# Kernel tuning notes

Measured on AMD Instinct MI355X. Metric: run time of the kernel, lower is better.

Reference implementation:

```python
import math
import jax, jax.numpy as jnp
import numpy as np

D_MODEL = 1024
N_HEADS = 16
D_K = D_MODEL // N_HEADS


def _build_neighbours(n_heads):
    # Mirrors LatticeMultiHeadAttention._build_neighbours for a (4,4)-style lattice.
    side = int(math.sqrt(n_heads))
    cols = side + 1 if side * side < n_heads else side
    positions = [divmod(i, cols) for i in range(n_heads)]
    pos_map = {p: j for j, p in enumerate(positions)}
    nb_idx = np.full((n_heads, 8), -1, dtype=np.int64)
    nb_w = np.zeros((n_heads, 8), dtype=np.float32)
    for i, (r, c) in enumerate(positions):
        k = 0
        for dr in (-1, 0, 1):
            for dc in (-1, 0, 1):
                if dr == 0 and dc == 0:
                    continue
                j = pos_map.get((r + dr, c + dc))
                if j is not None and k < 8:
                    nb_idx[i, k] = j
                    nb_w[i, k] = math.exp(-math.hypot(dr, dc))
                    k += 1
    return nb_idx, nb_w


def _phase_biases(coupling):
    # Sequential Kuramoto phase update: head h uses neighbor phases already
    # updated for heads < h (exactly as the torch per-head loop mutates buffers).
    H = coupling.shape[0]
    nb_idx, nb_w = _build_neighbours(H)
    phases = [jnp.asarray(0.0, coupling.dtype) for _ in range(H)]
    two_pi = 2.0 * math.pi
    for h in range(H):
        force = jnp.asarray(0.0, coupling.dtype)
        for k in range(8):
            j = int(nb_idx[h, k])
            if j >= 0:
                force = force + jnp.asarray(nb_w[h, k], coupling.dtype) * jnp.sin(phases[j] - phases[h])
        intrinsic = 1.0 + 0.1 * h
        new_phase = (phases[h] + 0.01 * (intrinsic + coupling[h] * force)) % two_pi
        phases[h] = new_phase
    return 0.1 * jnp.cos(jnp.stack(phases))  # [H] per-head scalar bias


def setup_inputs() -> dict:
    key = jax.random.key(0)
    ks = jax.random.split(key, 9)
    B, L = 2, 2048
    std = 0.02
    return {
        "query": jax.random.normal(ks[0], (B, L, D_MODEL), jnp.float32),
        "key": jax.random.normal(ks[1], (B, L, D_MODEL), jnp.float32),
        "value": jax.random.normal(ks[2], (B, L, D_MODEL), jnp.float32),
        "Wq": std * jax.random.normal(ks[3], (N_HEADS, D_MODEL, D_K), jnp.float32),
        "Wk": std * jax.random.normal(ks[4], (N_HEADS, D_MODEL, D_K), jnp.float32),
        "Wv": std * jax.random.normal(ks[5], (N_HEADS, D_MODEL, D_K), jnp.float32),
        "out_w": std * jax.random.normal(ks[6], (D_MODEL, D_MODEL), jnp.float32),
        "out_b": jnp.zeros((D_MODEL,), jnp.float32),
        "coupling": 0.1 * jnp.ones((N_HEADS,), jnp.float32),
    }


def reference(query, key, value, Wq, Wk, Wv, out_w, out_b, coupling):
    d_k = Wq.shape[-1]
    Q = jnp.einsum("bld,hdk->bhlk", query, Wq)
    K = jnp.einsum("bld,hdk->bhlk", key, Wk)
    V = jnp.einsum("bld,hdk->bhlk", value, Wv)
    scale = jnp.asarray(math.sqrt(float(d_k)), query.dtype)
    scores = jnp.einsum("bhlk,bhmk->bhlm", Q, K) / scale
    bias = _phase_biases(coupling)  # [H]
    scores = scores + bias[None, :, None, None]
    attn = jax.nn.softmax(scores, axis=-1)
    ctx = jnp.einsum("bhlm,bhmk->bhlk", attn, V)
    B, H, L, _ = ctx.shape
    out = ctx.transpose(0, 2, 1, 3).reshape(B, L, H * d_k)  # concat heads
    return out @ out_w + out_b
```

## Files before the change

kernel.cpp:

```cpp
#include <hip/hip_runtime.h>
#include <cstdint>

typedef uint16_t u16;
typedef __attribute__((ext_vector_type(8))) short bf16x8;
typedef __attribute__((ext_vector_type(4))) short bf16x4;
typedef __attribute__((ext_vector_type(4))) float f32x4;

#define QSCALE 0.18033688011112042f

struct Ptr3 { const float* a; const float* b; const float* c; };

__device__ __forceinline__ u16 f2bf(float x) {
  union { float f; uint32_t u; } v; v.f = x;
  uint32_t r = (v.u + 0x7fffu + ((v.u >> 16) & 1u)) >> 16;
  return (u16)r;
}

__device__ __forceinline__ void async16(void* lds, const void* g) {
  __builtin_amdgcn_global_load_lds((const __attribute__((address_space(1))) void*)g,
                                   (__attribute__((address_space(3))) void*)lds, 16, 0, 0);
}

__global__ __launch_bounds__(256) void k_cast3(Ptr3 in, u16* __restrict__ out) {
  const int z = blockIdx.y;
  const float* p = z == 0 ? in.a : (z == 1 ? in.b : in.c);
  int i = blockIdx.x * 256 + threadIdx.x;
  float4 v = ((const float4*)p)[i];
  bf16x4 o;
  o[0] = (short)f2bf(v.x); o[1] = (short)f2bf(v.y);
  o[2] = (short)f2bf(v.z); o[3] = (short)f2bf(v.w);
  *(bf16x4*)(out + (long)z * 4194304 + (long)i * 4) = o;
}

__global__ __launch_bounds__(256) void k_transpose_all(Ptr3 w, const float* __restrict__ ow,
                                                       u16* __restrict__ wt,
                                                       u16* __restrict__ wto) {
  __shared__ u16 tile[64 * 65];
  const int t = threadIdx.x;
  const int bx = blockIdx.x;
  const float* in;
  long in_base, out_base;
  int rstr, r0, c0;
  u16* outp;
  if (bx < 768) {
    int z = bx >> 4;
    r0 = (bx & 15) * 64; c0 = 0;
    in = (z < 16) ? w.a : (z < 32 ? w.b : w.c);
    in_base = (long)(z & 15) * 65536;
    out_base = (long)z * 65536;
    rstr = 64; outp = wt;
  } else {
    int idx = bx - 768;
    r0 = (idx >> 4) * 64; c0 = (idx & 15) * 64;
    in = ow; in_base = 0; out_base = 0;
    rstr = 1024; outp = wto;
  }
  for (int e = t; e < 4096; e += 256) {
    int rr = e >> 6, cc = e & 63;
    tile[rr * 65 + cc] = f2bf(in[in_base + (long)(r0 + rr) * rstr + c0 + cc]);
  }
  __syncthreads();
  for (int s = t; s < 512; s += 256) {
    int cc = s >> 3, r8 = (s & 7) << 3;
    bf16x8 p;
    #pragma unroll
    for (int j = 0; j < 8; ++j) p[j] = (short)tile[(r8 + j) * 65 + cc];
    *(bf16x8*)(outp + out_base + (long)(c0 + cc) * 1024 + r0 + r8) = p;
  }
}

__global__ __launch_bounds__(256) void k_gemm_qkv(const u16* __restrict__ A0,
                                                  const u16* __restrict__ B0,
                                                  u16* __restrict__ C0,
                                                  u16* __restrict__ Vt, float scale0) {
  __shared__ __align__(16) u16 As[128 * 32];
  __shared__ __align__(16) u16 Bs[128 * 32];
  __shared__ u16 T[128 * 130];
  const int z = blockIdx.z;
  const u16* A = A0 + (long)z * 4194304;
  const u16* Bt = B0 + (long)z * 1048576;
  const int t = threadIdx.x, lane = t & 63, quad = lane >> 4, l16 = lane & 15;
  const int wave = t >> 6, wy = wave >> 1, wx = wave & 1;
  const int m0 = blockIdx.y * 128, n0 = blockIdx.x * 128;
  const int wbase = t & 192;
  f32x4 acc[4][4] = {};
  for (int k0 = 0; k0 < 1024; k0 += 32) {
    __syncthreads();
    #pragma unroll
    for (int i = 0; i < 2; ++i) {
      int sb = i * 256 + wbase;
      int s = sb + lane;
      int row = s >> 2, c = s & 3;
      async16(As + sb * 8, A + (long)(m0 + row) * 1024 + k0 + c * 8);
      async16(Bs + sb * 8, Bt + (long)(n0 + row) * 1024 + k0 + c * 8);
    }
    __syncthreads();
    bf16x8 af[4], bfr[4];
    #pragma unroll
    for (int mt = 0; mt < 4; ++mt)
      af[mt] = *(const bf16x8*)(As + (wy * 64 + mt * 16 + l16) * 32 + quad * 8);
    #pragma unroll
    for (int nt = 0; nt < 4; ++nt)
      bfr[nt] = *(const bf16x8*)(Bs + (wx * 64 + nt * 16 + l16) * 32 + quad * 8);
    #pragma unroll
    for (int mt = 0; mt < 4; ++mt)
      #pragma unroll
      for (int nt = 0; nt < 4; ++nt)
        acc[mt][nt] = __builtin_amdgcn_mfma_f32_16x16x32_bf16(af[mt], bfr[nt], acc[mt][nt], 0, 0, 0);
  }
  if (z < 2) {
    u16* C = C0 + (long)z * 4194304;
    const float scale = z ? 1.0f : scale0;
    #pragma unroll
    for (int mt = 0; mt < 4; ++mt)
      #pragma unroll
      for (int nt = 0; nt < 4; ++nt) {
        int col = n0 + wx * 64 + nt * 16 + l16;
        #pragma unroll
        for (int r = 0; r < 4; ++r) {
          int row = m0 + wy * 64 + mt * 16 + quad * 4 + r;
          C[(long)row * 1024 + col] = f2bf(acc[mt][nt][r] * scale);
        }
      }
  } else {
    #pragma unroll
    for (int mt = 0; mt < 4; ++mt)
      #pragma unroll
      for (int nt = 0; nt < 4; ++nt) {
        int cc = wx * 64 + nt * 16 + l16;
        #pragma unroll
        for (int r = 0; r < 4; ++r)
          T[(wy * 64 + mt * 16 + quad * 4 + r) * 130 + cc] = f2bf(acc[mt][nt][r]);
      }
    __syncthreads();
    const int h0 = blockIdx.x * 2, bb = m0 >> 11, lb = m0 & 2047;
    #pragma unroll
    for (int i = 0; i < 8; ++i) {
      int s = t + i * 256;
      int c = s >> 4, l0 = (s & 15) * 8;
      bf16x8 p;
      #pragma unroll
      for (int j = 0; j < 8; ++j) p[j] = (short)T[(l0 + j) * 130 + c];
      *(bf16x8*)(Vt + (long)(bb * 16 + h0 + (c >> 6)) * 131072 +
                 (long)(c & 63) * 2048 + lb + l0) = p;
    }
  }
}

__global__ __launch_bounds__(256) void k_gemm_out(const u16* __restrict__ A,
                                                  const u16* __restrict__ Bt,
                                                  float* __restrict__ C,
                                                  const float* __restrict__ bias) {
  __shared__ __align__(16) u16 As[128 * 32];
  __shared__ __align__(16) u16 Bs[64 * 32];
  const int t = threadIdx.x, lane = t & 63, quad = lane >> 4, l16 = lane & 15;
  const int wave = t >> 6;
  const int m0 = blockIdx.y * 128, n0 = blockIdx.x * 64;
  const int wbase = t & 192;
  f32x4 acc[2][4] = {};
  for (int k0 = 0; k0 < 1024; k0 += 32) {
    __syncthreads();
    #pragma unroll
    for (int i = 0; i < 2; ++i) {
      int sb = i * 256 + wbase;
      int s = sb + lane;
      int row = s >> 2, c = s & 3;
      async16(As + sb * 8, A + (long)(m0 + row) * 1024 + k0 + c * 8);
    }
    {
      int s = t;
      int row = s >> 2, c = s & 3;
      async16(Bs + wbase * 8, Bt + (long)(n0 + row) * 1024 + k0 + c * 8);
    }
    __syncthreads();
    bf16x8 af[2], bfr[4];
    #pragma unroll
    for (int mt = 0; mt < 2; ++mt)
      af[mt] = *(const bf16x8*)(As + (wave * 32 + mt * 16 + l16) * 32 + quad * 8);
    #pragma unroll
    for (int nt = 0; nt < 4; ++nt)
      bfr[nt] = *(const bf16x8*)(Bs + (nt * 16 + l16) * 32 + quad * 8);
    #pragma unroll
    for (int mt = 0; mt < 2; ++mt)
      #pragma unroll
      for (int nt = 0; nt < 4; ++nt)
        acc[mt][nt] = __builtin_amdgcn_mfma_f32_16x16x32_bf16(af[mt], bfr[nt], acc[mt][nt], 0, 0, 0);
  }
  #pragma unroll
  for (int mt = 0; mt < 2; ++mt)
    #pragma unroll
    for (int nt = 0; nt < 4; ++nt) {
      int col = n0 + nt * 16 + l16;
      #pragma unroll
      for (int r = 0; r < 4; ++r) {
        int row = m0 + wave * 32 + mt * 16 + quad * 4 + r;
        C[(long)row * 1024 + col] = acc[mt][nt][r] + bias[col];
      }
    }
}

__global__ __launch_bounds__(512, 2) void k_flash(const u16* __restrict__ Qp,
                                                  const u16* __restrict__ Kp,
                                                  const u16* __restrict__ Vt,
                                                  u16* __restrict__ ctx) {
  __shared__ __align__(16) u16 qs[256 * 64];
  __shared__ __align__(16) u16 ks[64 * 72];
  __shared__ __align__(16) u16 vs[64 * 72];
  const int t = threadIdx.x, lane = t & 63, quad = lane >> 4, l16 = lane & 15;
  const int wave = t >> 6;
  const int bh = blockIdx.x & 31, b = bh >> 4, h = bh & 15;
  const int q0 = (blockIdx.x >> 5) * 256;
  const long gkbase = (long)b * 2097152 + h * 64;
  const long gvbase = (long)bh * 131072;
  const int srow = t >> 3, sc = t & 7;

  {
    long gq = (long)(b * 2048 + q0) * 1024 + h * 64;
    #pragma unroll
    for (int i = 0; i < 4; ++i) {
      int s = i * 512 + t;
      int row = s >> 3, pos = s & 7, c = pos ^ (row & 7);
      async16(qs + (long)s * 8, Qp + gq + (long)row * 1024 + c * 8);
    }
  }
  bf16x8 kreg = *(const bf16x8*)(Kp + gkbase + (long)srow * 1024 + sc * 8);
  bf16x8 vreg = *(const bf16x8*)(Vt + gvbase + (long)srow * 2048 + sc * 8);
  __syncthreads();

  bf16x8 qf[2][2];
  #pragma unroll
  for (int msub = 0; msub < 2; ++msub)
    #pragma unroll
    for (int kh = 0; kh < 2; ++kh) {
      int m = wave * 32 + msub * 16 + l16;
      int pos = (kh * 4 + quad) ^ (m & 7);
      qf[msub][kh] = *(const bf16x8*)(qs + m * 64 + pos * 8);
    }
  *(bf16x8*)(ks + srow * 72 + sc * 8) = kreg;
  *(bf16x8*)(vs + srow * 72 + sc * 8) = vreg;
  __syncthreads();

  u16* pw = qs + wave * 1152;

  float lsum[2][4] = {};
  f32x4 o[2][4] = {};

  for (int kt = 0; kt < 32; ++kt) {
    if (kt < 31) {
      int kv0 = (kt + 1) * 64;
      kreg = *(const bf16x8*)(Kp + gkbase + (long)(kv0 + srow) * 1024 + sc * 8);
      vreg = *(const bf16x8*)(Vt + gvbase + kv0 + (long)srow * 2048 + sc * 8);
    }

    bf16x8 kf[4][2], vf[4][2];
    #pragma unroll
    for (int nt = 0; nt < 4; ++nt)
      #pragma unroll
      for (int kh = 0; kh < 2; ++kh) {
        kf[nt][kh] = *(const bf16x8*)(ks + (nt * 16 + l16) * 72 + kh * 32 + quad * 8);
        vf[nt][kh] = *(const bf16x8*)(vs + (nt * 16 + l16) * 72 + kh * 32 + quad * 8);
      }

    #pragma unroll
    for (int msub = 0; msub < 2; ++msub) {
      #pragma unroll
      for (int nt = 0; nt < 4; ++nt) {
        f32x4 a = {};
        #pragma unroll
        for (int kh = 0; kh < 2; ++kh)
          a = __builtin_amdgcn_mfma_f32_16x16x32_bf16(qf[msub][kh], kf[nt][kh], a, 0, 0, 0);
        #pragma unroll
        for (int r = 0; r < 4; ++r) {
          float e = __builtin_amdgcn_exp2f(a[r]);
          lsum[msub][r] += e;
          pw[(quad * 4 + r) * 72 + nt * 16 + l16] = f2bf(e);
        }
      }
      #pragma unroll
      for (int kh = 0; kh < 2; ++kh) {
        bf16x8 pa = *(const bf16x8*)(pw + l16 * 72 + kh * 32 + quad * 8);
        #pragma unroll
        for (int nt = 0; nt < 4; ++nt)
          o[msub][nt] = __builtin_amdgcn_mfma_f32_16x16x32_bf16(pa, vf[nt][kh], o[msub][nt], 0, 0, 0);
      }
    }

    __syncthreads();
    if (kt < 31) {
      *(bf16x8*)(ks + srow * 72 + sc * 8) = kreg;
      *(bf16x8*)(vs + srow * 72 + sc * 8) = vreg;
    }
    __syncthreads();
  }

  #pragma unroll
  for (int msub = 0; msub < 2; ++msub)
    #pragma unroll
    for (int r = 0; r < 4; ++r) {
      float l = lsum[msub][r];
      #pragma unroll
      for (int d = 1; d < 16; d <<= 1) l += __shfl_xor(l, d);
      lsum[msub][r] = 1.0f / l;
    }
  #pragma unroll
  for (int msub = 0; msub < 2; ++msub)
    #pragma unroll
    for (int nt = 0; nt < 4; ++nt)
      #pragma unroll
      for (int r = 0; r < 4; ++r) {
        int q = q0 + wave * 32 + msub * 16 + quad * 4 + r;
        long idx = (long)(b * 2048 + q) * 1024 + h * 64 + nt * 16 + l16;
        ctx[idx] = f2bf(o[msub][nt][r] * lsum[msub][r]);
      }
}

extern "C" void kernel_launch(void* const* d_in, const int* in_sizes, int n_in,
                              void* d_out, int out_size, void* d_ws, size_t ws_size,
                              hipStream_t stream) {
  const float* query = (const float*)d_in[0];
  const float* key   = (const float*)d_in[1];
  const float* value = (const float*)d_in[2];
  const float* Wq    = (const float*)d_in[3];
  const float* Wk    = (const float*)d_in[4];
  const float* Wv    = (const float*)d_in[5];
  const float* out_w = (const float*)d_in[6];
  const float* out_b = (const float*)d_in[7];
  float* out = (float*)d_out;

  char* ws = (char*)d_ws;
  size_t off = 0;
  auto alloc = [&](size_t bytes) {
    void* p = ws + off;
    off += (bytes + 255) & ~(size_t)255;
    return p;
  };
  u16* qb  = (u16*)alloc(4096L * 1024 * 2);
  u16* kb  = (u16*)alloc(4096L * 1024 * 2);
  u16* vb  = (u16*)alloc(4096L * 1024 * 2);
  u16* wtq = (u16*)alloc(1024L * 1024 * 2);
  u16* wtk = (u16*)alloc(1024L * 1024 * 2);
  u16* wtv = (u16*)alloc(1024L * 1024 * 2);
  u16* wto = (u16*)alloc(1024L * 1024 * 2);
  u16* Qp  = (u16*)alloc(4096L * 1024 * 2);
  u16* Kp  = (u16*)alloc(4096L * 1024 * 2);
  u16* Vtb = (u16*)alloc(4096L * 1024 * 2);
  u16* ctx = qb;
  (void)kb; (void)vb; (void)wtk; (void)wtv; (void)Kp;

  k_cast3<<<dim3(4096, 3), 256, 0, stream>>>(Ptr3{query, key, value}, qb);

  k_transpose_all<<<1024, 256, 0, stream>>>(Ptr3{Wq, Wk, Wv}, out_w, wtq, wto);

  k_gemm_qkv<<<dim3(8, 32, 3), 256, 0, stream>>>(qb, wtq, Qp, Vtb, QSCALE);

  k_flash<<<256, 512, 0, stream>>>(Qp, Kp, Vtb, ctx);

  k_gemm_out<<<dim3(16, 32), 256, 0, stream>>>(ctx, wto, out, out_b);
}
```

Baseline: 246.3 us.

## Merge prep kernels, widen QKV GEMM k-tile with XOR swizzle, use packed bf16 conversion

Merges the input cast and weight transpose into one prep launch to cut a kernel launch. The QKV GEMM now stages a k-depth of 64 per iteration with an XOR-swizzled LDS layout, which halves barrier count and avoids bank conflicts. Its LDS buffers are shared with the transpose scratch area, which needs an extra barrier. Float-to-bf16 conversion uses the hardware packed-convert builtin when it is available, in the GEMM epilogues, the flash softmax P write and the ctx store. Risk: the packed convert's rounding may differ slightly from the manual round-to-nearest-even code.

New measurement: 234.4 us. 1.05x faster.

```diff
diff --git a/kernel.cpp b/kernel.cpp
--- a/kernel.cpp
+++ b/kernel.cpp
@@ -16,48 +16,63 @@
   return (u16)r;
 }
 
+#if __has_builtin(__builtin_amdgcn_cvt_pk_bf16_f32)
+typedef __bf16 bf2_t __attribute__((ext_vector_type(2)));
+__device__ __forceinline__ uint32_t pkbf(float a, float b) {
+  bf2_t v = __builtin_amdgcn_cvt_pk_bf16_f32(a, b);
+  uint32_t u;
+  __builtin_memcpy(&u, &v, 4);
+  return u;
+}
+#else
+__device__ __forceinline__ uint32_t pkbf(float a, float b) {
+  return (uint32_t)f2bf(a) | ((uint32_t)f2bf(b) << 16);
+}
+#endif
+
 __device__ __forceinline__ void async16(void* lds, const void* g) {
   __builtin_amdgcn_global_load_lds((const __attribute__((address_space(1))) void*)g,
                                    (__attribute__((address_space(3))) void*)lds, 16, 0, 0);
 }
 
-__global__ __launch_bounds__(256) void k_cast3(Ptr3 in, u16* __restrict__ out) {
-  const int z = blockIdx.y;
-  const float* p = z == 0 ? in.a : (z == 1 ? in.b : in.c);
-  int i = blockIdx.x * 256 + threadIdx.x;
-  float4 v = ((const float4*)p)[i];
-  bf16x4 o;
-  o[0] = (short)f2bf(v.x); o[1] = (short)f2bf(v.y);
-  o[2] = (short)f2bf(v.z); o[3] = (short)f2bf(v.w);
-  *(bf16x4*)(out + (long)z * 4194304 + (long)i * 4) = o;
-}
-
-__global__ __launch_bounds__(256) void k_transpose_all(Ptr3 w, const float* __restrict__ ow,
-                                                       u16* __restrict__ wt,
-                                                       u16* __restrict__ wto) {
+__global__ __launch_bounds__(256) void k_prep(Ptr3 in, u16* __restrict__ out,
+                                              Ptr3 w, const float* __restrict__ ow,
+                                              u16* __restrict__ wt, u16* __restrict__ wto) {
   __shared__ u16 tile[64 * 65];
   const int t = threadIdx.x;
   const int bx = blockIdx.x;
-  const float* in;
+  if (bx < 12288) {
+    int z = bx >> 12;
+    int i = (bx & 4095) * 256 + t;
+    const float* p = z == 0 ? in.a : (z == 1 ? in.b : in.c);
+    float4 v = ((const float4*)p)[i];
+    uint2 o2;
+    o2.x = pkbf(v.x, v.y);
+    o2.y = pkbf(v.z, v.w);
+    *(uint2*)(out + (long)z * 4194304 + (long)i * 4) = o2;
+    return;
+  }
+  const int b2 = bx - 12288;
+  const float* src;
   long in_base, out_base;
   int rstr, r0, c0;
   u16* outp;
-  if (bx < 768) {
-    int z = bx >> 4;
-    r0 = (bx & 15) * 64; c0 = 0;
-    in = (z < 16) ? w.a : (z < 32 ? w.b : w.c);
+  if (b2 < 768) {
+    int z = b2 >> 4;
+    r0 = (b2 & 15) * 64; c0 = 0;
+    src = (z < 16) ? w.a : (z < 32 ? w.b : w.c);
     in_base = (long)(z & 15) * 65536;
     out_base = (long)z * 65536;
     rstr = 64; outp = wt;
   } else {
-    int idx = bx - 768;
+    int idx = b2 - 768;
     r0 = (idx >> 4) * 64; c0 = (idx & 15) * 64;
-    in = ow; in_base = 0; out_base = 0;
+    src = ow; in_base = 0; out_base = 0;
     rstr = 1024; outp = wto;
   }
   for (int e = t; e < 4096; e += 256) {
     int rr = e >> 6, cc = e & 63;
-    tile[rr * 65 + cc] = f2bf(in[in_base + (long)(r0 + rr) * rstr + c0 + cc]);
+    tile[rr * 65 + cc] = f2bf(src[in_base + (long)(r0 + rr) * rstr + c0 + cc]);
   }
   __syncthreads();
   for (int s = t; s < 512; s += 256) {
@@ -73,9 +88,10 @@
                                                   const u16* __restrict__ B0,
                                                   u16* __restrict__ C0,
                                                   u16* __restrict__ Vt, float scale0) {
-  __shared__ __align__(16) u16 As[128 * 32];
-  __shared__ __align__(16) u16 Bs[128 * 32];
-  __shared__ u16 T[128 * 130];
+  __shared__ __align__(16) u16 smem[16640];
+  u16* As = smem;
+  u16* Bs = smem + 8192;
+  u16* T  = smem;
   const int z = blockIdx.z;
   const u16* A = A0 + (long)z * 4194304;
   const u16* Bt = B0 + (long)z * 1048576;
@@ -84,29 +100,39 @@
   const int m0 = blockIdx.y * 128, n0 = blockIdx.x * 128;
   const int wbase = t & 192;
   f32x4 acc[4][4] = {};
-  for (int k0 = 0; k0 < 1024; k0 += 32) {
-    __syncthreads();
-    #pragma unroll
-    for (int i = 0; i < 2; ++i) {
+  for (int k0 = 0; k0 < 1024; k0 += 64) {
+    __syncthreads();
+    #pragma unroll
+    for (int i = 0; i < 4; ++i) {
       int sb = i * 256 + wbase;
       int s = sb + lane;
-      int row = s >> 2, c = s & 3;
-      async16(As + sb * 8, A + (long)(m0 + row) * 1024 + k0 + c * 8);
-      async16(Bs + sb * 8, Bt + (long)(n0 + row) * 1024 + k0 + c * 8);
-    }
-    __syncthreads();
-    bf16x8 af[4], bfr[4];
-    #pragma unroll
-    for (int mt = 0; mt < 4; ++mt)
-      af[mt] = *(const bf16x8*)(As + (wy * 64 + mt * 16 + l16) * 32 + quad * 8);
-    #pragma unroll
-    for (int nt = 0; nt < 4; ++nt)
-      bfr[nt] = *(const bf16x8*)(Bs + (wx * 64 + nt * 16 + l16) * 32 + quad * 8);
-    #pragma unroll
-    for (int mt = 0; mt < 4; ++mt)
-      #pragma unroll
-      for (int nt = 0; nt < 4; ++nt)
-        acc[mt][nt] = __builtin_amdgcn_mfma_f32_16x16x32_bf16(af[mt], bfr[nt], acc[mt][nt], 0, 0, 0);
+      int row = s >> 3, c = s & 7;
+      int cs = c ^ (row & 7);
+      async16(As + sb * 8, A + (long)(m0 + row) * 1024 + k0 + cs * 8);
+      async16(Bs + sb * 8, Bt + (long)(n0 + row) * 1024 + k0 + cs * 8);
+    }
+    __syncthreads();
+    #pragma unroll
+    for (int kk = 0; kk < 2; ++kk) {
+      bf16x8 af[4], bfr[4];
+      #pragma unroll
+      for (int mt = 0; mt < 4; ++mt) {
+        int row = wy * 64 + mt * 16 + l16;
+        int pos = (kk * 4 + quad) ^ (row & 7);
+        af[mt] = *(const bf16x8*)(As + row * 64 + pos * 8);
+      }
+      #pragma unroll
+      for (int nt = 0; nt < 4; ++nt) {
+        int row = wx * 64 + nt * 16 + l16;
+        int pos = (kk * 4 + quad) ^ (row & 7);
+        bfr[nt] = *(const bf16x8*)(Bs + row * 64 + pos * 8);
+      }
+      #pragma unroll
+      for (int mt = 0; mt < 4; ++mt)
+        #pragma unroll
+        for (int nt = 0; nt < 4; ++nt)
+          acc[mt][nt] = __builtin_amdgcn_mfma_f32_16x16x32_bf16(af[mt], bfr[nt], acc[mt][nt], 0, 0, 0);
+    }
   }
   if (z < 2) {
     u16* C = C0 + (long)z * 4194304;
@@ -116,21 +142,28 @@
       #pragma unroll
       for (int nt = 0; nt < 4; ++nt) {
         int col = n0 + wx * 64 + nt * 16 + l16;
-        #pragma unroll
-        for (int r = 0; r < 4; ++r) {
-          int row = m0 + wy * 64 + mt * 16 + quad * 4 + r;
-          C[(long)row * 1024 + col] = f2bf(acc[mt][nt][r] * scale);
-        }
+        int row = m0 + wy * 64 + mt * 16 + quad * 4;
+        uint32_t ua = pkbf(acc[mt][nt][0] * scale, acc[mt][nt][1] * scale);
+        uint32_t ub = pkbf(acc[mt][nt][2] * scale, acc[mt][nt][3] * scale);
+        C[(long)row * 1024 + col] = (u16)ua;
+        C[(long)(row + 1) * 1024 + col] = (u16)(ua >> 16);
+        C[(long)(row + 2) * 1024 + col] = (u16)ub;
+        C[(long)(row + 3) * 1024 + col] = (u16)(ub >> 16);
       }
   } else {
+    __syncthreads();
     #pragma unroll
     for (int mt = 0; mt < 4; ++mt)
       #pragma unroll
       for (int nt = 0; nt < 4; ++nt) {
         int cc = wx * 64 + nt * 16 + l16;
-        #pragma unroll
-        for (int r = 0; r < 4; ++r)
-          T[(wy * 64 + mt * 16 + quad * 4 + r) * 130 + cc] = f2bf(acc[mt][nt][r]);
+        int rr = wy * 64 + mt * 16 + quad * 4;
+        uint32_t ua = pkbf(acc[mt][nt][0], acc[mt][nt][1]);
+        uint32_t ub = pkbf(acc[mt][nt][2], acc[mt][nt][3]);
+        T[(rr + 0) * 130 + cc] = (u16)ua;
+        T[(rr + 1) * 130 + cc] = (u16)(ua >> 16);
+        T[(rr + 2) * 130 + cc] = (u16)ub;
+        T[(rr + 3) * 130 + cc] = (u16)(ub >> 16);
       }
     __syncthreads();
     const int h0 = blockIdx.x * 2, bb = m0 >> 11, lb = m0 & 2047;
@@ -269,12 +302,18 @@
         #pragma unroll
         for (int kh = 0; kh < 2; ++kh)
           a = __builtin_amdgcn_mfma_f32_16x16x32_bf16(qf[msub][kh], kf[nt][kh], a, 0, 0, 0);
-        #pragma unroll
-        for (int r = 0; r < 4; ++r) {
-          float e = __builtin_amdgcn_exp2f(a[r]);
-          lsum[msub][r] += e;
-          pw[(quad * 4 + r) * 72 + nt * 16 + l16] = f2bf(e);
-        }
+        float e0 = __builtin_amdgcn_exp2f(a[0]);
+        float e1 = __builtin_amdgcn_exp2f(a[1]);
+        float e2 = __builtin_amdgcn_exp2f(a[2]);
+        float e3 = __builtin_amdgcn_exp2f(a[3]);
+        lsum[msub][0] += e0; lsum[msub][1] += e1;
+        lsum[msub][2] += e2; lsum[msub][3] += e3;
+        uint32_t ua = pkbf(e0, e1), ub = pkbf(e2, e3);
+        u16* pc = pw + (quad * 4) * 72 + nt * 16 + l16;
+        pc[0]       = (u16)ua;
+        pc[72]      = (u16)(ua >> 16);
+        pc[144]     = (u16)ub;
+        pc[216]     = (u16)(ub >> 16);
       }
       #pragma unroll
       for (int kh = 0; kh < 2; ++kh) {
@@ -305,13 +344,16 @@
   #pragma unroll
   for (int msub = 0; msub < 2; ++msub)
     #pragma unroll
-    for (int nt = 0; nt < 4; ++nt)
-      #pragma unroll
-      for (int r = 0; r < 4; ++r) {
-        int q = q0 + wave * 32 + msub * 16 + quad * 4 + r;
-        long idx = (long)(b * 2048 + q) * 1024 + h * 64 + nt * 16 + l16;
-        ctx[idx] = f2bf(o[msub][nt][r] * lsum[msub][r]);
-      }
+    for (int nt = 0; nt < 4; ++nt) {
+      int q = q0 + wave * 32 + msub * 16 + quad * 4;
+      long idx = (long)(b * 2048 + q) * 1024 + h * 64 + nt * 16 + l16;
+      uint32_t ua = pkbf(o[msub][nt][0] * lsum[msub][0], o[msub][nt][1] * lsum[msub][1]);
+      uint32_t ub = pkbf(o[msub][nt][2] * lsum[msub][2], o[msub][nt][3] * lsum[msub][3]);
+      ctx[idx]        = (u16)ua;
+      ctx[idx + 1024] = (u16)(ua >> 16);
+      ctx[idx + 2048] = (u16)ub;
+      ctx[idx + 3072] = (u16)(ub >> 16);
+    }
 }
 
 extern "C" void kernel_launch(void* const* d_in, const int* in_sizes, int n_in,
@@ -347,9 +389,8 @@
   u16* ctx = qb;
   (void)kb; (void)vb; (void)wtk; (void)wtv; (void)Kp;
 
-  k_cast3<<<dim3(4096, 3), 256, 0, stream>>>(Ptr3{query, key, value}, qb);
-
-  k_transpose_all<<<1024, 256, 0, stream>>>(Ptr3{Wq, Wk, Wv}, out_w, wtq, wto);
+  k_prep<<<13312, 256, 0, stream>>>(Ptr3{query, key, value}, qb,
+                                    Ptr3{Wq, Wk, Wv}, out_w, wtq, wto);
 
   k_gemm_qkv<<<dim3(8, 32, 3), 256, 0, stream>>>(qb, wtq, Qp, Vtb, QSCALE);
 
```
